# Performance work log

Hardware: AMD Instinct MI355X
Metric: run time of the kernel (lower is better)

The kernel has to match this reference:

```python
import jax, jax.numpy as jnp
import numpy as np

B, LV, D = 8, 4096, 256   # batch, temporal length, channels
N = 2048                   # total ROIs across the batch
P = 32                     # output_size (number of output bins)
G = int(np.ceil(LV / P))   # static max adaptive sampling grid (sampling_ratio=-1)


def setup_inputs() -> dict:
    key = jax.random.key(0)
    k1, k2, k3 = jax.random.split(key, 3)
    feat = jax.random.normal(k1, (B, LV, D), dtype=jnp.float32)
    # boxes: (start, end) along the lv axis, sorted so start <= end, in [0, LV)
    boxes = jnp.sort(
        jax.random.uniform(k2, (N, 2), dtype=jnp.float32, minval=0.0, maxval=float(LV)),
        axis=1,
    )
    batch_idx = jax.random.randint(k3, (N,), 0, B, dtype=jnp.int32)
    return {"feat": feat, "boxes": boxes, "batch_idx": batch_idx}


def _roi_align_1d(feat, boxes, batch_idx):
    # Faithful 1D specialization of torchvision roi_align with boxes
    # (0, y1, 1, y2), output_size=(P, 1), aligned=True, spatial_scale=1,
    # sampling_ratio=-1. The width axis contributes a single sample at x=0
    # with weight 1, so only the y (lv) axis math remains.
    feat_flat = feat.reshape(B * LV, D)
    y1, y2 = boxes[:, 0], boxes[:, 1]
    roi_h = y2 - y1                       # aligned=True: no max(., 1) clamp
    start = y1 - 0.5                      # aligned offset
    bin_h = roi_h / P                     # [N]
    grid_h = jnp.ceil(bin_h).astype(jnp.int32)          # adaptive samples per bin
    count = jnp.maximum(grid_h, 1).astype(feat.dtype)   # avg denominator
    sub = bin_h / jnp.maximum(grid_h, 1)                # spacing inside a bin [N]
    # bin start positions: [N, P]
    bin_off = start[:, None] + jnp.arange(P, dtype=feat.dtype)[None, :] * bin_h[:, None]
    base = batch_idx.astype(jnp.int32) * LV             # [N] row offset into feat_flat

    def bilinear(y):  # y: [N, P] -> [N, P, D]
        valid = (y >= -1.0) & (y <= float(LV))
        yc = jnp.maximum(y, 0.0)
        y_lo = jnp.floor(yc).astype(jnp.int32)
        hi_case = y_lo >= LV - 1
        y_lo = jnp.where(hi_case, LV - 1, y_lo)
        y_hi = jnp.where(hi_case, LV - 1, y_lo + 1)
        yc = jnp.where(hi_case, y_lo.astype(y.dtype), yc)
        ly = yc - y_lo.astype(y.dtype)
        v = (1.0 - ly)[..., None] * feat_flat[base[:, None] + y_lo] \
            + ly[..., None] * feat_flat[base[:, None] + y_hi]
        return jnp.where(valid[..., None], v, 0.0)

    def step(acc, g):
        y = bin_off + (g.astype(feat.dtype) + 0.5) * sub[:, None]   # [N, P]
        m = (g < grid_h)[:, None, None]                              # sample active?
        return acc + jnp.where(m, bilinear(y), 0.0), None

    acc0 = jnp.zeros((N, P, D), dtype=feat.dtype)
    acc, _ = jax.lax.scan(step, acc0, jnp.arange(G, dtype=jnp.int32))
    return acc / count[:, None, None]   # [N, P, D] (torch output after transpose(1,2))


def reference(feat, boxes, batch_idx):
    return _roi_align_1d(feat, boxes, batch_idx)
```

## Files before the change

### kernel.cpp

```cpp
#include <hip/hip_runtime.h>

#define B_    8
#define LV_   4096
#define D_    256
#define N_    2048
#define P_    32
#define WROWS_ 64
#define NWIN_  (B_ * (LV_ / WROWS_))
#define NBINS_ (N_ * P_)
#define CPB_   32

typedef float v4f __attribute__((ext_vector_type(4)));

__device__ __forceinline__ float lane_bcast_f(float v, int l) {
    return __int_as_float(__builtin_amdgcn_readlane(__float_as_int(v), l));
}

__device__ __forceinline__ int bin_r_first(const float* __restrict__ boxes, int n, int p) {
    const float y1 = boxes[2 * n], y2 = boxes[2 * n + 1];
    const float bin_h = (y2 - y1) * (1.0f / (float)P_);
    const int gh = (int)ceilf(bin_h);
    if (gh < 1) return 0;
    const float sub  = bin_h / (float)gh;
    const float boff = (y1 - 0.5f) + (float)p * bin_h;
    const float a    = fmaf(0.5f, sub, boff);
    int r = (int)floorf(a);
    if (r < 0) r = 0;
    if (r > LV_ - 1) r = LV_ - 1;
    return r;
}

__device__ __forceinline__ int bin_key(const float* __restrict__ boxes,
                                       const int* __restrict__ batch_idx, int idx) {
    const int n = idx >> 5, p = idx & 31;
    return (batch_idx[n] << 6) | (bin_r_first(boxes, n, p) >> 6);
}

__global__ __launch_bounds__(256) void count_bins_kernel(
    const float* __restrict__ boxes, const int* __restrict__ batch_idx,
    int* __restrict__ cnt)
{
    const int idx = blockIdx.x * 256 + threadIdx.x;
    atomicAdd(&cnt[bin_key(boxes, batch_idx, idx)], 1);
}

__global__ __launch_bounds__(NWIN_) void scan_kernel(int* __restrict__ cnt)
{
    __shared__ int s[NWIN_];
    const int t = threadIdx.x;
    s[t] = cnt[t];
    __syncthreads();
    for (int off = 1; off < NWIN_; off <<= 1) {
        const int v = (t >= off) ? s[t - off] : 0;
        __syncthreads();
        s[t] += v;
        __syncthreads();
    }
    cnt[t] = (t == 0) ? 0 : s[t - 1];
}

__global__ __launch_bounds__(256) void scatter_bins_kernel(
    const float* __restrict__ boxes, const int* __restrict__ batch_idx,
    int* __restrict__ cnt, int* __restrict__ binlist)
{
    const int idx = blockIdx.x * 256 + threadIdx.x;
    binlist[atomicAdd(&cnt[bin_key(boxes, batch_idx, idx)], 1)] = idx;
}

__global__ __launch_bounds__(256) void build_order_kernel(
    const int* __restrict__ batch_idx, int* __restrict__ order)
{
    __shared__ int cnt[B_], cur[B_];
    const int tid = threadIdx.x;
    if (tid < B_) cnt[tid] = 0;
    __syncthreads();
    for (int n = tid; n < N_; n += 256) atomicAdd(&cnt[batch_idx[n]], 1);
    __syncthreads();
    if (tid == 0) { int s = 0; for (int b = 0; b < B_; ++b) { cur[b] = s; s += cnt[b]; } }
    __syncthreads();
    for (int n = tid; n < N_; n += 256)
        order[atomicAdd(&cur[batch_idx[n]], 1)] = n;
}

__global__ __launch_bounds__(256) void roi_rows_kernel(
    const float* __restrict__ feat, const float* __restrict__ boxes,
    const int* __restrict__ batch_idx, const int* __restrict__ order,
    float* __restrict__ out)
{
    const int nwg = (N_ * P_) / 4;
    const int cpx = nwg >> 3;
    const int bid = blockIdx.x;
    const int swz = (bid & 7) * cpx + (bid >> 3);
    const int slot = (swz << 2) + (threadIdx.x >> 6);
    const int n    = __builtin_amdgcn_readfirstlane(order[slot >> 5]);
    const int p    = slot & (P_ - 1);
    const int lane = threadIdx.x & 63;
    const int bi   = __builtin_amdgcn_readfirstlane(batch_idx[n]);
    const float y1 = boxes[2 * n], y2 = boxes[2 * n + 1];
    const float bin_h = (y2 - y1) * (1.0f / (float)P_);
    const int gh = (int)ceilf(bin_h);
    const v4f* prow = (const v4f*)feat + (long)bi * (LV_ * (D_ / 4));
    v4f acc0 = {0.f,0.f,0.f,0.f}, acc1 = {0.f,0.f,0.f,0.f};
    if (gh >= 1) {
        const float cntf = (float)gh, sub = bin_h / cntf, inv_sub = 1.0f / sub;
        const float halfsub = 0.5f * sub;
        const float boff = (y1 - 0.5f) + (float)p * bin_h;
        const float a = fmaf(0.5f, sub, boff), ylast = fmaf(cntf - 0.5f, sub, boff);
        int r_first = (int)floorf(a);
        if (r_first < 0) r_first = 0; if (r_first > LV_-1) r_first = LV_-1;
        int r_last = (int)floorf(ylast) + 1;
        if (r_last > LV_-1) r_last = LV_-1; if (r_last < r_first) r_last = r_first;
        const int r0 = __builtin_amdgcn_readfirstlane(r_first);
        const int rl = __builtin_amdgcn_readfirstlane(r_last);
        const float lanef = (float)lane;
        for (int base = r0; base <= rl; base += 64) {
            int kmax = rl - base; if (kmax > 63) kmax = 63;
            const int r = base + lane;
            const float d0 = ((float)base + lanef) - a;
            const float dm = d0 - 1.0f, dp = d0 + 1.0f;
            const float nm = fminf(fmaxf(ceilf(dm * inv_sub), 0.0f), cntf);
            const float n0 = fminf(fmaxf(ceilf(d0 * inv_sub), 0.0f), cntf);
            const float np = fminf(fmaxf(ceilf(dp * inv_sub), 0.0f), cntf);
            float Pm = fmaf(nm, dm, -halfsub * fmaf(nm, nm, -nm));
            float P0 = fmaf(n0, d0, -halfsub * fmaf(n0, n0, -n0));
            float Pp = fmaf(np, dp, -halfsub * fmaf(np, np, -np));
            if (r == 0)       Pm = P0;
            if (r == LV_ - 1) Pp = P0 + cntf;
            const float Wl = (Pm + Pp) - 2.0f * P0;
            const v4f* pS = prow + (long)base * (D_ / 4);
            int k = 0;
            for (; k + 4 <= kmax + 1; k += 4) {
                v4f v0 = pS[lane], v1 = pS[lane+64], v2 = pS[lane+128], v3 = pS[lane+192];
                acc0 += v0 * lane_bcast_f(Wl, k);   acc1 += v1 * lane_bcast_f(Wl, k+1);
                acc0 += v2 * lane_bcast_f(Wl, k+2); acc1 += v3 * lane_bcast_f(Wl, k+3);
                pS += 4 * (D_ / 4);
            }
            for (; k <= kmax; ++k) { v4f v = pS[lane]; acc0 += v * lane_bcast_f(Wl, k); pS += (D_ / 4); }
        }
    }
    const float inv_c = 1.0f / (float)(gh > 1 ? gh : 1);
    v4f res = (acc0 + acc1) * inv_c;
    v4f* op = (v4f*)out + ((long)n * P_ + p) * (D_ / 4) + lane;
    __builtin_nontemporal_store(res, op);
}

__global__ __launch_bounds__(512) void roi_win_kernel(
    const float* __restrict__ feat, const float* __restrict__ boxes,
    const int* __restrict__ batch_idx, const int* __restrict__ binlist,
    float* __restrict__ out)
{
    __shared__ v4f tile[WROWS_ * 64];
    const int nblk = NBINS_ / CPB_;
    const int bid  = blockIdx.x;
    const int blk  = (bid & 7) * (nblk >> 3) + (bid >> 3);
    const int tid  = threadIdx.x;
    const int lane = tid & 63;
    const int wv   = tid >> 6;

    const int idx0 = binlist[blk * CPB_];
    const int wb   = __builtin_amdgcn_readfirstlane(batch_idx[idx0 >> 5]);
    const int wlo  = __builtin_amdgcn_readfirstlane(
                         (bin_r_first(boxes, idx0 >> 5, idx0 & 31) >> 6) << 6);

    {
        const int r0 = wv * 8;
        const float* srow = feat + ((long)wb * LV_ + wlo + r0) * D_ + lane * 4;
        v4f* lrow = tile + r0 * 64;
#if __has_builtin(__builtin_amdgcn_global_load_lds)
        #pragma unroll
        for (int j = 0; j < 8; ++j) {
            __builtin_amdgcn_global_load_lds(
                (const __attribute__((address_space(1))) void*)(srow + j * D_),
                (__attribute__((address_space(3))) void*)(lrow + j * 64),
                16, 0, 0);
        }
#else
        const v4f* src = (const v4f*)feat + ((long)wb * LV_ + wlo + r0) * (D_ / 4) + lane;
        v4f t0 = src[0],   t1 = src[64],  t2 = src[128], t3 = src[192];
        v4f t4 = src[256], t5 = src[320], t6 = src[384], t7 = src[448];
        v4f* dst = lrow + lane;
        dst[0]   = t0; dst[64]  = t1; dst[128] = t2; dst[192] = t3;
        dst[256] = t4; dst[320] = t5; dst[384] = t6; dst[448] = t7;
#endif
    }
    __syncthreads();

    for (int i = wv; i < CPB_; i += 8) {
        const int idx = __builtin_amdgcn_readfirstlane(binlist[blk * CPB_ + i]);
        const int n = idx >> 5, p = idx & 31;
        const int bi = __builtin_amdgcn_readfirstlane(batch_idx[n]);

        const float y1 = boxes[2 * n], y2 = boxes[2 * n + 1];
        const float bin_h = (y2 - y1) * (1.0f / (float)P_);
        const int gh = (int)ceilf(bin_h);

        const v4f* prow = (const v4f*)feat + (long)bi * (LV_ * (D_ / 4));
        v4f acc0 = {0.f,0.f,0.f,0.f}, acc1 = {0.f,0.f,0.f,0.f};

        if (gh >= 1) {
            const float cntf = (float)gh, sub = bin_h / cntf, inv_sub = 1.0f / sub;
            const float halfsub = 0.5f * sub;
            const float boff = (y1 - 0.5f) + (float)p * bin_h;
            const float a = fmaf(0.5f, sub, boff), ylast = fmaf(cntf - 0.5f, sub, boff);

            int r_first = (int)floorf(a);
            if (r_first < 0) r_first = 0; if (r_first > LV_-1) r_first = LV_-1;
            int r_last = (int)floorf(ylast) + 1;
            if (r_last > LV_-1) r_last = LV_-1; if (r_last < r_first) r_last = r_first;
            const int r0 = __builtin_amdgcn_readfirstlane(r_first);
            const int rl = __builtin_amdgcn_readfirstlane(r_last);
            const float lanef = (float)lane;

            for (int gbase = r0; gbase <= rl; gbase += 64) {
                int kmax = rl - gbase; if (kmax > 63) kmax = 63;

                const int   r  = gbase + lane;
                const float d0 = ((float)gbase + lanef) - a;
                const float dm = d0 - 1.0f, dp = d0 + 1.0f;
                const float nm = fminf(fmaxf(ceilf(dm * inv_sub), 0.0f), cntf);
                const float n0 = fminf(fmaxf(ceilf(d0 * inv_sub), 0.0f), cntf);
                const float np = fminf(fmaxf(ceilf(dp * inv_sub), 0.0f), cntf);
                float Pm = fmaf(nm, dm, -halfsub * fmaf(nm, nm, -nm));
                float P0 = fmaf(n0, d0, -halfsub * fmaf(n0, n0, -n0));
                float Pp = fmaf(np, dp, -halfsub * fmaf(np, np, -np));
                if (r == 0)       Pm = P0;
                if (r == LV_ - 1) Pp = P0 + cntf;
                const float Wl = (Pm + Pp) - 2.0f * P0;

                const int t = kmax + 1;
                int lo, hi;
                if (bi == wb) {
                    lo = wlo - gbase;          lo = lo < 0 ? 0 : (lo > t ? t : lo);
                    hi = wlo + WROWS_ - gbase; hi = hi < lo ? lo : (hi > t ? t : hi);
                } else { lo = t; hi = t; }

#define GSEG(KS, KE) do {                                                        \
    int k = (KS);                                                                \
    const v4f* pS = prow + (long)(gbase + k) * (D_ / 4);                         \
    for (; k + 4 <= (KE); k += 4) {                                              \
        v4f v0 = pS[lane], v1 = pS[lane+64], v2 = pS[lane+128], v3 = pS[lane+192];\
        acc0 += v0 * lane_bcast_f(Wl, k);   acc1 += v1 * lane_bcast_f(Wl, k+1);  \
        acc0 += v2 * lane_bcast_f(Wl, k+2); acc1 += v3 * lane_bcast_f(Wl, k+3);  \
        pS += 4 * (D_ / 4); }                                                    \
    for (; k < (KE); ++k) { v4f v = pS[lane]; acc0 += v * lane_bcast_f(Wl, k); pS += (D_ / 4); } \
} while (0)

                GSEG(0, lo);
                {
                    int k = lo;
                    const v4f* tp = tile + (gbase + lo - wlo) * 64 + lane;
                    for (; k + 4 <= hi; k += 4) {
                        v4f t0 = tp[0], t1 = tp[64], t2 = tp[128], t3 = tp[192];
                        acc0 += t0 * lane_bcast_f(Wl, k);   acc1 += t1 * lane_bcast_f(Wl, k+1);
                        acc0 += t2 * lane_bcast_f(Wl, k+2); acc1 += t3 * lane_bcast_f(Wl, k+3);
                        tp += 256;
                    }
                    for (; k < hi; ++k) { acc0 += tp[0] * lane_bcast_f(Wl, k); tp += 64; }
                }
                GSEG(hi, t);
#undef GSEG
            }
        }

        const float inv_c = 1.0f / (float)(gh > 1 ? gh : 1);
        v4f res = (acc0 + acc1) * inv_c;
        v4f* op = (v4f*)out + ((long)n * P_ + p) * (D_ / 4) + lane;
        __builtin_nontemporal_store(res, op);
    }
}

extern "C" void kernel_launch(void* const* d_in, const int* in_sizes, int n_in,
                              void* d_out, int out_size, void* d_ws, size_t ws_size,
                              hipStream_t stream) {
    const float* feat      = (const float*)d_in[0];
    const float* boxes     = (const float*)d_in[1];
    const int*   batch_idx = (const int*)d_in[2];
    float*       out       = (float*)d_out;

    if (ws_size >= (size_t)(NBINS_ + NWIN_) * sizeof(int)) {
        int* binlist = (int*)d_ws;
        int* cnt     = binlist + NBINS_;
        hipMemsetAsync(cnt, 0, NWIN_ * sizeof(int), stream);
        count_bins_kernel<<<NBINS_ / 256, 256, 0, stream>>>(boxes, batch_idx, cnt);
        scan_kernel<<<1, NWIN_, 0, stream>>>(cnt);
        scatter_bins_kernel<<<NBINS_ / 256, 256, 0, stream>>>(boxes, batch_idx, cnt, binlist);
        roi_win_kernel<<<NBINS_ / CPB_, 512, 0, stream>>>(feat, boxes, batch_idx, binlist, out);
    } else {
        int* order = (int*)d_ws;
        build_order_kernel<<<1, 256, 0, stream>>>(batch_idx, order);
        roi_rows_kernel<<<(N_ * P_) / 4, 256, 0, stream>>>(feat, boxes, batch_idx, order, out);
    }
}
```

Before: 212.5 us.

## Replace count-scan-scatter binning with fixed-capacity per-window buckets and overflow list

Drops the count and prefix-scan kernels and scatters bins straight into fixed-capacity buckets, one per 64-row window, with an overflow list for buckets that fill up. The window kernel now launches a fixed grid of window-segment blocks that exit early when their segment is empty, plus extra blocks that process overflow bins from global memory. This removes two kernel launches and a serial dependency, at the cost of many empty blocks, possibly partial 32-bin segments that under-use the tile, and a larger workspace requirement. The per-bin math is moved into a shared helper.

```diff
diff --git a/kernel.cpp b/kernel.cpp
--- a/kernel.cpp
+++ b/kernel.cpp
@@ -1,14 +1,18 @@
 #include <hip/hip_runtime.h>
 
-#define B_    8
-#define LV_   4096
-#define D_    256
-#define N_    2048
-#define P_    32
+#define B_     8
+#define LV_    4096
+#define D_     256
+#define N_     2048
+#define P_     32
 #define WROWS_ 64
 #define NWIN_  (B_ * (LV_ / WROWS_))
 #define NBINS_ (N_ * P_)
+#define CAP_   256
 #define CPB_   32
+#define SEGS_  (CAP_ / CPB_)
+#define NGW_   (NWIN_ * SEGS_)
+#define NOVF_  64
 
 typedef float v4f __attribute__((ext_vector_type(4)));
 
@@ -30,82 +34,43 @@
     return r;
 }
 
-__device__ __forceinline__ int bin_key(const float* __restrict__ boxes,
-                                       const int* __restrict__ batch_idx, int idx) {
-    const int n = idx >> 5, p = idx & 31;
-    return (batch_idx[n] << 6) | (bin_r_first(boxes, n, p) >> 6);
-}
-
-__global__ __launch_bounds__(256) void count_bins_kernel(
-    const float* __restrict__ boxes, const int* __restrict__ batch_idx,
-    int* __restrict__ cnt)
-{
-    const int idx = blockIdx.x * 256 + threadIdx.x;
-    atomicAdd(&cnt[bin_key(boxes, batch_idx, idx)], 1);
-}
-
-__global__ __launch_bounds__(NWIN_) void scan_kernel(int* __restrict__ cnt)
-{
-    __shared__ int s[NWIN_];
-    const int t = threadIdx.x;
-    s[t] = cnt[t];
-    __syncthreads();
-    for (int off = 1; off < NWIN_; off <<= 1) {
-        const int v = (t >= off) ? s[t - off] : 0;
-        __syncthreads();
-        s[t] += v;
-        __syncthreads();
-    }
-    cnt[t] = (t == 0) ? 0 : s[t - 1];
-}
-
 __global__ __launch_bounds__(256) void scatter_bins_kernel(
     const float* __restrict__ boxes, const int* __restrict__ batch_idx,
-    int* __restrict__ cnt, int* __restrict__ binlist)
-{
+    int* __restrict__ wsp)
+{
+    int* cnt    = wsp;
+    int* ovfc   = wsp + NWIN_;
+    int* bucket = wsp + 1024;
+    int* ovf    = bucket + NWIN_ * CAP_;
     const int idx = blockIdx.x * 256 + threadIdx.x;
-    binlist[atomicAdd(&cnt[bin_key(boxes, batch_idx, idx)], 1)] = idx;
-}
-
-__global__ __launch_bounds__(256) void build_order_kernel(
-    const int* __restrict__ batch_idx, int* __restrict__ order)
-{
-    __shared__ int cnt[B_], cur[B_];
-    const int tid = threadIdx.x;
-    if (tid < B_) cnt[tid] = 0;
-    __syncthreads();
-    for (int n = tid; n < N_; n += 256) atomicAdd(&cnt[batch_idx[n]], 1);
-    __syncthreads();
-    if (tid == 0) { int s = 0; for (int b = 0; b < B_; ++b) { cur[b] = s; s += cnt[b]; } }
-    __syncthreads();
-    for (int n = tid; n < N_; n += 256)
-        order[atomicAdd(&cur[batch_idx[n]], 1)] = n;
-}
-
-__global__ __launch_bounds__(256) void roi_rows_kernel(
+    const int n = idx >> 5, p = idx & 31;
+    const int key = (batch_idx[n] << 6) | (bin_r_first(boxes, n, p) >> 6);
+    const int slot = atomicAdd(&cnt[key], 1);
+    if (slot < CAP_) bucket[key * CAP_ + slot] = idx;
+    else             ovf[atomicAdd(ovfc, 1)] = idx;
+}
+
+__device__ __forceinline__ void process_bin(
     const float* __restrict__ feat, const float* __restrict__ boxes,
-    const int* __restrict__ batch_idx, const int* __restrict__ order,
-    float* __restrict__ out)
-{
-    const int nwg = (N_ * P_) / 4;
-    const int cpx = nwg >> 3;
-    const int bid = blockIdx.x;
-    const int swz = (bid & 7) * cpx + (bid >> 3);
-    const int slot = (swz << 2) + (threadIdx.x >> 6);
-    const int n    = __builtin_amdgcn_readfirstlane(order[slot >> 5]);
-    const int p    = slot & (P_ - 1);
-    const int lane = threadIdx.x & 63;
-    const int bi   = __builtin_amdgcn_readfirstlane(batch_idx[n]);
+    const int* __restrict__ batch_idx, float* __restrict__ out,
+    const v4f* tile, int wb, int wlo, int idx, int lane)
+{
+    const int n = idx >> 5, p = idx & 31;
+    const int bi = __builtin_amdgcn_readfirstlane(batch_idx[n]);
+
     const float y1 = boxes[2 * n], y2 = boxes[2 * n + 1];
     const float bin_h = (y2 - y1) * (1.0f / (float)P_);
     const int gh = (int)ceilf(bin_h);
+
     const v4f* prow = (const v4f*)feat + (long)bi * (LV_ * (D_ / 4));
     v4f acc0 = {0.f,0.f,0.f,0.f}, acc1 = {0.f,0.f,0.f,0.f};
+
     if (gh >= 1) {
         const float cntf = (float)gh, sub = bin_h / cntf, inv_sub = 1.0f / sub;
         const float halfsub = 0.5f * sub;
         const float boff = (y1 - 0.5f) + (float)p * bin_h;
         const float a = fmaf(0.5f, sub, boff), ylast = fmaf(cntf - 0.5f, sub, boff);
+
         int r_first = (int)floorf(a);
         if (r_first < 0) r_first = 0; if (r_first > LV_-1) r_first = LV_-1;
         int r_last = (int)floorf(ylast) + 1;
@@ -113,10 +78,12 @@
         const int r0 = __builtin_amdgcn_readfirstlane(r_first);
         const int rl = __builtin_amdgcn_readfirstlane(r_last);
         const float lanef = (float)lane;
-        for (int base = r0; base <= rl; base += 64) {
-            int kmax = rl - base; if (kmax > 63) kmax = 63;
-            const int r = base + lane;
-            const float d0 = ((float)base + lanef) - a;
+
+        for (int gbase = r0; gbase <= rl; gbase += 64) {
+            int kmax = rl - gbase; if (kmax > 63) kmax = 63;
+
+            const int   r  = gbase + lane;
+            const float d0 = ((float)gbase + lanef) - a;
             const float dm = d0 - 1.0f, dp = d0 + 1.0f;
             const float nm = fminf(fmaxf(ceilf(dm * inv_sub), 0.0f), cntf);
             const float n0 = fminf(fmaxf(ceilf(d0 * inv_sub), 0.0f), cntf);
@@ -127,17 +94,42 @@
             if (r == 0)       Pm = P0;
             if (r == LV_ - 1) Pp = P0 + cntf;
             const float Wl = (Pm + Pp) - 2.0f * P0;
-            const v4f* pS = prow + (long)base * (D_ / 4);
-            int k = 0;
-            for (; k + 4 <= kmax + 1; k += 4) {
-                v4f v0 = pS[lane], v1 = pS[lane+64], v2 = pS[lane+128], v3 = pS[lane+192];
-                acc0 += v0 * lane_bcast_f(Wl, k);   acc1 += v1 * lane_bcast_f(Wl, k+1);
-                acc0 += v2 * lane_bcast_f(Wl, k+2); acc1 += v3 * lane_bcast_f(Wl, k+3);
-                pS += 4 * (D_ / 4);
+
+            const int t = kmax + 1;
+            int lo, hi;
+            if (tile && bi == wb) {
+                lo = wlo - gbase;          lo = lo < 0 ? 0 : (lo > t ? t : lo);
+                hi = wlo + WROWS_ - gbase; hi = hi < lo ? lo : (hi > t ? t : hi);
+            } else { lo = t; hi = t; }
+
+#define GSEG(KS, KE) do {                                                        \
+    int k = (KS);                                                                \
+    const v4f* pS = prow + (long)(gbase + k) * (D_ / 4);                         \
+    for (; k + 4 <= (KE); k += 4) {                                              \
+        v4f v0 = pS[lane], v1 = pS[lane+64], v2 = pS[lane+128], v3 = pS[lane+192];\
+        acc0 += v0 * lane_bcast_f(Wl, k);   acc1 += v1 * lane_bcast_f(Wl, k+1);  \
+        acc0 += v2 * lane_bcast_f(Wl, k+2); acc1 += v3 * lane_bcast_f(Wl, k+3);  \
+        pS += 4 * (D_ / 4); }                                                    \
+    for (; k < (KE); ++k) { v4f v = pS[lane]; acc0 += v * lane_bcast_f(Wl, k); pS += (D_ / 4); } \
+} while (0)
+
+            GSEG(0, lo);
+            {
+                int k = lo;
+                const v4f* tp = tile + (gbase + lo - wlo) * 64 + lane;
+                for (; k + 4 <= hi; k += 4) {
+                    v4f t0 = tp[0], t1 = tp[64], t2 = tp[128], t3 = tp[192];
+                    acc0 += t0 * lane_bcast_f(Wl, k);   acc1 += t1 * lane_bcast_f(Wl, k+1);
+                    acc0 += t2 * lane_bcast_f(Wl, k+2); acc1 += t3 * lane_bcast_f(Wl, k+3);
+                    tp += 256;
+                }
+                for (; k < hi; ++k) { acc0 += tp[0] * lane_bcast_f(Wl, k); tp += 64; }
             }
-            for (; k <= kmax; ++k) { v4f v = pS[lane]; acc0 += v * lane_bcast_f(Wl, k); pS += (D_ / 4); }
+            GSEG(hi, t);
+#undef GSEG
         }
     }
+
     const float inv_c = 1.0f / (float)(gh > 1 ? gh : 1);
     v4f res = (acc0 + acc1) * inv_c;
     v4f* op = (v4f*)out + ((long)n * P_ + p) * (D_ / 4) + lane;
@@ -146,21 +138,40 @@
 
 __global__ __launch_bounds__(512) void roi_win_kernel(
     const float* __restrict__ feat, const float* __restrict__ boxes,
-    const int* __restrict__ batch_idx, const int* __restrict__ binlist,
+    const int* __restrict__ batch_idx, const int* __restrict__ wsp,
     float* __restrict__ out)
 {
     __shared__ v4f tile[WROWS_ * 64];
-    const int nblk = NBINS_ / CPB_;
-    const int bid  = blockIdx.x;
-    const int blk  = (bid & 7) * (nblk >> 3) + (bid >> 3);
+    const int* cnt    = wsp;
+    const int* ovfc   = wsp + NWIN_;
+    const int* bucket = wsp + 1024;
+    const int* ovf    = bucket + NWIN_ * CAP_;
+
     const int tid  = threadIdx.x;
     const int lane = tid & 63;
     const int wv   = tid >> 6;
-
-    const int idx0 = binlist[blk * CPB_];
-    const int wb   = __builtin_amdgcn_readfirstlane(batch_idx[idx0 >> 5]);
-    const int wlo  = __builtin_amdgcn_readfirstlane(
-                         (bin_r_first(boxes, idx0 >> 5, idx0 & 31) >> 6) << 6);
+    const int bid  = blockIdx.x;
+
+    if (bid >= NGW_) {
+        const int no = ovfc[0];
+        for (int j = (bid - NGW_) * 8 + wv; j < no; j += NOVF_ * 8) {
+            const int idx = __builtin_amdgcn_readfirstlane(ovf[j]);
+            process_bin(feat, boxes, batch_idx, out, nullptr, 0, 0, idx, lane);
+        }
+        return;
+    }
+
+    const int blk = (bid & 7) * (NGW_ / 8) + (bid >> 3);
+    const int w   = blk >> 3;
+    const int seg = blk & (SEGS_ - 1);
+
+    const int total = min(cnt[w], CAP_);
+    const int start = seg * CPB_;
+    if (start >= total) return;
+    const int nb = min(CPB_, total - start);
+
+    const int wb  = w >> 6;
+    const int wlo = (w & 63) << 6;
 
     {
         const int r0 = wv * 8;
@@ -185,88 +196,41 @@
     }
     __syncthreads();
 
-    for (int i = wv; i < CPB_; i += 8) {
-        const int idx = __builtin_amdgcn_readfirstlane(binlist[blk * CPB_ + i]);
-        const int n = idx >> 5, p = idx & 31;
-        const int bi = __builtin_amdgcn_readfirstlane(batch_idx[n]);
-
-        const float y1 = boxes[2 * n], y2 = boxes[2 * n + 1];
-        const float bin_h = (y2 - y1) * (1.0f / (float)P_);
-        const int gh = (int)ceilf(bin_h);
-
-        const v4f* prow = (const v4f*)feat + (long)bi * (LV_ * (D_ / 4));
-        v4f acc0 = {0.f,0.f,0.f,0.f}, acc1 = {0.f,0.f,0.f,0.f};
-
-        if (gh >= 1) {
-            const float cntf = (float)gh, sub = bin_h / cntf, inv_sub = 1.0f / sub;
-            const float halfsub = 0.5f * sub;
-            const float boff = (y1 - 0.5f) + (float)p * bin_h;
-            const float a = fmaf(0.5f, sub, boff), ylast = fmaf(cntf - 0.5f, sub, boff);
-
-            int r_first = (int)floorf(a);
-            if (r_first < 0) r_first = 0; if (r_first > LV_-1) r_first = LV_-1;
-            int r_last = (int)floorf(ylast) + 1;
-            if (r_last > LV_-1) r_last = LV_-1; if (r_last < r_first) r_last = r_first;
-            const int r0 = __builtin_amdgcn_readfirstlane(r_first);
-            const int rl = __builtin_amdgcn_readfirstlane(r_last);
-            const float lanef = (float)lane;
-
-            for (int gbase = r0; gbase <= rl; gbase += 64) {
-                int kmax = rl - gbase; if (kmax > 63) kmax = 63;
-
-                const int   r  = gbase + lane;
-                const float d0 = ((float)gbase + lanef) - a;
-                const float dm = d0 - 1.0f, dp = d0 + 1.0f;
-                const float nm = fminf(fmaxf(ceilf(dm * inv_sub), 0.0f), cntf);
-                const float n0 = fminf(fmaxf(ceilf(d0 * inv_sub), 0.0f), cntf);
-                const float np = fminf(fmaxf(ceilf(dp * inv_sub), 0.0f), cntf);
-                float Pm = fmaf(nm, dm, -halfsub * fmaf(nm, nm, -nm));
-                float P0 = fmaf(n0, d0, -halfsub * fmaf(n0, n0, -n0));
-                float Pp = fmaf(np, dp, -halfsub * fmaf(np, np, -np));
-                if (r == 0)       Pm = P0;
-                if (r == LV_ - 1) Pp = P0 + cntf;
-                const float Wl = (Pm + Pp) - 2.0f * P0;
-
-                const int t = kmax + 1;
-                int lo, hi;
-                if (bi == wb) {
-                    lo = wlo - gbase;          lo = lo < 0 ? 0 : (lo > t ? t : lo);
-                    hi = wlo + WROWS_ - gbase; hi = hi < lo ? lo : (hi > t ? t : hi);
-                } else { lo = t; hi = t; }
-
-#define GSEG(KS, KE) do {                                                        \
-    int k = (KS);                                                                \
-    const v4f* pS = prow + (long)(gbase + k) * (D_ / 4);                         \
-    for (; k + 4 <= (KE); k += 4) {                                              \
-        v4f v0 = pS[lane], v1 = pS[lane+64], v2 = pS[lane+128], v3 = pS[lane+192];\
-        acc0 += v0 * lane_bcast_f(Wl, k);   acc1 += v1 * lane_bcast_f(Wl, k+1);  \
-        acc0 += v2 * lane_bcast_f(Wl, k+2); acc1 += v3 * lane_bcast_f(Wl, k+3);  \
-        pS += 4 * (D_ / 4); }                                                    \
-    for (; k < (KE); ++k) { v4f v = pS[lane]; acc0 += v * lane_bcast_f(Wl, k); pS += (D_ / 4); } \
-} while (0)
-
-                GSEG(0, lo);
-                {
-                    int k = lo;
-                    const v4f* tp = tile + (gbase + lo - wlo) * 64 + lane;
-                    for (; k + 4 <= hi; k += 4) {
-                        v4f t0 = tp[0], t1 = tp[64], t2 = tp[128], t3 = tp[192];
-                        acc0 += t0 * lane_bcast_f(Wl, k);   acc1 += t1 * lane_bcast_f(Wl, k+1);
-                        acc0 += t2 * lane_bcast_f(Wl, k+2); acc1 += t3 * lane_bcast_f(Wl, k+3);
-                        tp += 256;
-                    }
-                    for (; k < hi; ++k) { acc0 += tp[0] * lane_bcast_f(Wl, k); tp += 64; }
-                }
-                GSEG(hi, t);
-#undef GSEG
-            }
-        }
-
-        const float inv_c = 1.0f / (float)(gh > 1 ? gh : 1);
-        v4f res = (acc0 + acc1) * inv_c;
-        v4f* op = (v4f*)out + ((long)n * P_ + p) * (D_ / 4) + lane;
-        __builtin_nontemporal_store(res, op);
-    }
+    for (int i = wv; i < nb; i += 8) {
+        const int idx = __builtin_amdgcn_readfirstlane(bucket[w * CAP_ + start + i]);
+        process_bin(feat, boxes, batch_idx, out, tile, wb, wlo, idx, lane);
+    }
+}
+
+__global__ __launch_bounds__(256) void build_order_kernel(
+    const int* __restrict__ batch_idx, int* __restrict__ order)
+{
+    __shared__ int cnt[B_], cur[B_];
+    const int tid = threadIdx.x;
+    if (tid < B_) cnt[tid] = 0;
+    __syncthreads();
+    for (int n = tid; n < N_; n += 256) atomicAdd(&cnt[batch_idx[n]], 1);
+    __syncthreads();
+    if (tid == 0) { int s = 0; for (int b = 0; b < B_; ++b) { cur[b] = s; s += cnt[b]; } }
+    __syncthreads();
+    for (int n = tid; n < N_; n += 256)
+        order[atomicAdd(&cur[batch_idx[n]], 1)] = n;
+}
+
+__global__ __launch_bounds__(256) void roi_rows_kernel(
+    const float* __restrict__ feat, const float* __restrict__ boxes,
+    const int* __restrict__ batch_idx, const int* __restrict__ order,
+    float* __restrict__ out)
+{
+    const int nwg = (N_ * P_) / 4;
+    const int cpx = nwg >> 3;
+    const int bid = blockIdx.x;
+    const int swz = (bid & 7) * cpx + (bid >> 3);
+    const int slot = (swz << 2) + (threadIdx.x >> 6);
+    const int n    = __builtin_amdgcn_readfirstlane(order[slot >> 5]);
+    const int p    = slot & (P_ - 1);
+    const int lane = threadIdx.x & 63;
+    process_bin(feat, boxes, batch_idx, out, nullptr, 0, 0, (n << 5) | p, lane);
 }
 
 extern "C" void kernel_launch(void* const* d_in, const int* in_sizes, int n_in,
@@ -277,14 +241,12 @@
     const int*   batch_idx = (const int*)d_in[2];
     float*       out       = (float*)d_out;
 
-    if (ws_size >= (size_t)(NBINS_ + NWIN_) * sizeof(int)) {
-        int* binlist = (int*)d_ws;
-        int* cnt     = binlist + NBINS_;
-        hipMemsetAsync(cnt, 0, NWIN_ * sizeof(int), stream);
-        count_bins_kernel<<<NBINS_ / 256, 256, 0, stream>>>(boxes, batch_idx, cnt);
-        scan_kernel<<<1, NWIN_, 0, stream>>>(cnt);
-        scatter_bins_kernel<<<NBINS_ / 256, 256, 0, stream>>>(boxes, batch_idx, cnt, binlist);
-        roi_win_kernel<<<NBINS_ / CPB_, 512, 0, stream>>>(feat, boxes, batch_idx, binlist, out);
+    const size_t need = (size_t)(1024 + NWIN_ * CAP_ + NBINS_) * sizeof(int);
+    if (ws_size >= need) {
+        int* wsp = (int*)d_ws;
+        hipMemsetAsync(wsp, 0, (NWIN_ + 1) * sizeof(int), stream);
+        scatter_bins_kernel<<<NBINS_ / 256, 256, 0, stream>>>(boxes, batch_idx, wsp);
+        roi_win_kernel<<<NGW_ + NOVF_, 512, 0, stream>>>(feat, boxes, batch_idx, wsp, out);
     } else {
         int* order = (int*)d_ws;
         build_order_kernel<<<1, 256, 0, stream>>>(batch_idx, order);
```

Measured after the change: 222.2 us. +4.5%, slower.
